# Optimization experiments

Hardware: AMD Instinct MI355X
Metric: run time of the kernel (lower is better)

Reference implementation:

```python
import jax, jax.numpy as jnp
import numpy as np

B, C, T, V = 8, 64, 16, 207
H, WSZ = 8, 4
EPS = 1e-5


def setup_inputs() -> dict:
    key = jax.random.key(0)
    ks = jax.random.split(key, 16)
    def w(k, shape):
        return jax.random.normal(k, shape, jnp.float32) * 0.02
    inp = {"x": jax.random.normal(ks[0], (B, C, T, V), jnp.float32)}
    for i, s in enumerate("ab"):
        o = 1 + i * 4
        inp[f"qkv_w_{s}"] = w(ks[o], (C, 3 * C))
        inp[f"qkv_b_{s}"] = jnp.zeros((3 * C,), jnp.float32)
        inp[f"proj_w_{s}"] = w(ks[o + 1], (C, C))
        inp[f"proj_b_{s}"] = jnp.zeros((C,), jnp.float32)
        inp[f"ffn_w1_{s}"] = w(ks[o + 2], (C, 4 * C))
        inp[f"ffn_b1_{s}"] = jnp.zeros((4 * C,), jnp.float32)
        inp[f"ffn_w2_{s}"] = w(ks[o + 3], (4 * C, C))
        inp[f"ffn_b2_{s}"] = jnp.zeros((C,), jnp.float32)
        inp[f"ln_{s}1_g"] = jnp.ones((C, T, V), jnp.float32)
        inp[f"ln_{s}1_b"] = jnp.zeros((C, T, V), jnp.float32)
        inp[f"ln_{s}2_g"] = jnp.ones((C, T, V), jnp.float32)
        inp[f"ln_{s}2_b"] = jnp.zeros((C, T, V), jnp.float32)
    inp["n_head"] = H
    inp["window_size"] = WSZ
    return inp


def _layer_norm(x, g, b):
    # LayerNorm over (C, T, V) dims of [B, C, T, V]
    mu = jnp.mean(x, axis=(1, 2, 3), keepdims=True)
    var = jnp.var(x, axis=(1, 2, 3), keepdims=True)
    return (x - mu) / jnp.sqrt(var + EPS) * g + b


def _window_att(x, wqkv, bqkv, wo, bo, n_head, wsz):
    # Joint spatio-temporal attention within windows of `wsz` timesteps.
    b_, c_, t_, v_ = x.shape
    nw = t_ // wsz
    dh = c_ // n_head
    # [B,C,T,V] -> [B,T,V,C] -> [B,nW, wsz*V, C]
    xt = jnp.transpose(x, (0, 2, 3, 1)).reshape(b_, nw, wsz * v_, c_)
    qkv = xt @ wqkv + bqkv  # [B,nW,N,3C]
    q, k, v = jnp.split(qkv, 3, axis=-1)
    def heads(t):
        return t.reshape(b_, nw, -1, n_head, dh).transpose(0, 1, 3, 2, 4)  # [B,nW,H,N,dh]
    q, k, v = heads(q), heads(k), heads(v)
    scale = 1.0 / jnp.sqrt(jnp.asarray(dh, jnp.float32))
    att = jax.nn.softmax(jnp.einsum('bwhnd,bwhmd->bwhnm', q, k) * scale, axis=-1)
    out = jnp.einsum('bwhnm,bwhmd->bwhnd', att, v)
    out = out.transpose(0, 1, 3, 2, 4).reshape(b_, nw, wsz * v_, c_) @ wo + bo
    return out.reshape(b_, t_, v_, c_).transpose(0, 3, 1, 2)


def _ffn(x, w1, b1, w2, b2):
    h = jax.nn.relu(jnp.einsum('bctv,cd->bdtv', x, w1) + b1[None, :, None, None])
    return jnp.einsum('bdtv,dc->bctv', h, w2) + b2[None, :, None, None]


def _block(x, wqkv, bqkv, wo, bo, w1, b1, w2, b2, g1, be1, g2, be2, n_head, wsz):
    x = _window_att(x, wqkv, bqkv, wo, bo, n_head, wsz) + x
    x = _layer_norm(x, g1, be1)
    x = _ffn(x, w1, b1, w2, b2) + x
    x = _layer_norm(x, g2, be2)
    # cyclic shift along time by shift_pixel = wsz // 2
    return jnp.roll(x, -(wsz // 2), axis=2)


def reference(x, qkv_w_a, qkv_b_a, proj_w_a, proj_b_a, ffn_w1_a, ffn_b1_a, ffn_w2_a, ffn_b2_a,
              ln_a1_g, ln_a1_b, ln_a2_g, ln_a2_b,
              qkv_w_b, qkv_b_b, proj_w_b, proj_b_b, ffn_w1_b, ffn_b1_b, ffn_w2_b, ffn_b2_b,
              ln_b1_g, ln_b1_b, ln_b2_g, ln_b2_b, n_head, window_size):
    x = _block(x, qkv_w_a, qkv_b_a, proj_w_a, proj_b_a, ffn_w1_a, ffn_b1_a, ffn_w2_a, ffn_b2_a,
               ln_a1_g, ln_a1_b, ln_a2_g, ln_a2_b, n_head, window_size)
    x = _block(x, qkv_w_b, qkv_b_b, proj_w_b, proj_b_b, ffn_w1_b, ffn_b1_b, ffn_w2_b, ffn_b2_b,
               ln_b1_g, ln_b1_b, ln_b2_g, ln_b2_b, n_head, window_size)
    return x
```

## Files before the change

kernel.cpp:

```cpp
#include <hip/hip_runtime.h>
#include <hip/hip_bf16.h>

#define Bb  8
#define Cc  64
#define Tt  16
#define Vv  207
#define Hh  8
#define DH  8
#define NW  4
#define WSZ 4
#define Nn  (WSZ*Vv)
#define NP  832
#define TV  (Tt*Vv)
#define CTV (Cc*Tt*Vv)
#define S   (Bb*CTV)
#define NBWH (Bb*NW*Hh)
#define EPSF 1e-5f
#define QSCALE 0.51006971401146f
#define FRAG_BWH (52*64*4)
#define LAYER_WSZ 49152

typedef __attribute__((ext_vector_type(4))) short bf16x4;
typedef __attribute__((ext_vector_type(4))) float f32x4;
typedef __attribute__((ext_vector_type(2))) unsigned int u32x2;

static __device__ __forceinline__ short f2bf(float f) {
    union { float f; unsigned u; } v; v.f = f;
    unsigned r = (v.u + 0x7FFFu + ((v.u >> 16) & 1u)) >> 16;
    return (short)r;
}

static __device__ __forceinline__ bf16x4 pack4(float a, float b, float c, float d) {
    unsigned ua = __builtin_bit_cast(unsigned, a) + 0x8000u;
    unsigned ub = __builtin_bit_cast(unsigned, b) + 0x8000u;
    unsigned uc = __builtin_bit_cast(unsigned, c) + 0x8000u;
    unsigned ud = __builtin_bit_cast(unsigned, d) + 0x8000u;
    u32x2 t;
    t[0] = (ua >> 16) | (ub & 0xFFFF0000u);
    t[1] = (uc >> 16) | (ud & 0xFFFF0000u);
    return __builtin_bit_cast(bf16x4, t);
}

static __device__ __forceinline__ float pexp2(float x) {
    float t = __builtin_fmaf(x, 0.0558263f, 0.2401536f);
    t = __builtin_fmaf(x, t, 0.6931471f);
    return __builtin_fmaf(x, t, 1.0f);
}

__global__ void prep_w_kernel(const float* __restrict__ qa, const float* __restrict__ pa,
                              const float* __restrict__ w1a, const float* __restrict__ w2a,
                              const float* __restrict__ qbw, const float* __restrict__ pbw,
                              const float* __restrict__ w1b, const float* __restrict__ w2b,
                              short* __restrict__ wf, float* __restrict__ stats) {
    if (blockIdx.x == 0 && threadIdx.x < 64) stats[threadIdx.x] = 0.f;
    int i = blockIdx.x*256 + threadIdx.x;
    int l = i / 12288; int f = i % 12288;
    const float* qw = l ? qbw : qa;
    const float* pw = l ? pbw : pa;
    const float* w1 = l ? w1b : w1a;
    const float* w2 = l ? w2b : w2a;
    short* dst = wf + l*LAYER_WSZ;
    bf16x4 out;
    if (f < 3072) {
        int s = f; int nt = s>>8; int kc = (s>>6)&3; int ln = s&63;
        int li = ln&15; int q = ln>>4;
        #pragma unroll
        for (int j = 0; j < 4; ++j) out[j] = f2bf(qw[(kc*16+q*4+j)*192 + nt*16+li]);
        *((bf16x4*)&dst[s*4]) = out;
    } else if (f < 4096) {
        int s = f-3072; int nt = s>>8; int kc = (s>>6)&3; int ln = s&63;
        int li = ln&15; int q = ln>>4;
        #pragma unroll
        for (int j = 0; j < 4; ++j) out[j] = f2bf(pw[(kc*16+q*4+j)*64 + nt*16+li]);
        *((bf16x4*)&dst[12288 + s*4]) = out;
    } else if (f < 8192) {
        int s = f-4096; int nt = s>>8; int kc = (s>>6)&3; int ln = s&63;
        int li = ln&15; int q = ln>>4;
        #pragma unroll
        for (int j = 0; j < 4; ++j) out[j] = f2bf(w1[(kc*16+q*4+j)*256 + nt*16+li]);
        *((bf16x4*)&dst[16384 + s*4]) = out;
    } else {
        int s = f-8192; int nt = s>>8; int ct = (s>>6)&3; int ln = s&63;
        int li = ln&15; int q = ln>>4;
        #pragma unroll
        for (int j = 0; j < 4; ++j) out[j] = f2bf(w2[(nt*16+q*4+j)*64 + ct*16+li]);
        *((bf16x4*)&dst[32768 + s*4]) = out;
    }
}

__global__ void prep_pads_kernel(short* __restrict__ qf, short* __restrict__ kf,
                                 short* __restrict__ vf) {
    for (int i = blockIdx.x*256 + threadIdx.x; i < NBWH*1664; i += 416*256) {
        int bwh = i / 1664; int rest = i % 1664;
        int nt = rest >> 5; int u = rest & 31;
        size_t base = (size_t)bwh*FRAG_BWH + nt*256;
        *((u32x2*)&qf[base + (32+u)*4]) = (u32x2){0u,0u};
        *((u32x2*)&kf[base + (32+u)*4]) = (u32x2){0u,0u};
        int vlane = (u>>3)*16 + 8 + (u&7);
        short v = ((u&7) == 0) ? (short)0x3F80 : (short)0;
        bf16x4 vv4 = {v,v,v,v};
        *((bf16x4*)&vf[base + vlane*4]) = vv4;
    }
}

__global__ __launch_bounds__(256) void qkv_kernel(const float* __restrict__ src,
        const float* __restrict__ st, const float* __restrict__ g, const float* __restrict__ be,
        const short* __restrict__ wfq, const float* __restrict__ bias,
        short* __restrict__ qf, short* __restrict__ kf, short* __restrict__ vf) {
    __shared__ short wqs[12288];
    __shared__ float bqs[192];
    __shared__ short os[64*196];
    int tid = threadIdx.x;
    int b = blockIdx.x / 52;
    int r0 = (blockIdx.x % 52) * 64;
    const float* xb = src + (size_t)b*CTV;
    {
        const u32x2* wsrc = (const u32x2*)wfq;
        u32x2* wdst = (u32x2*)wqs;
        for (int s = tid; s < 3072; s += 256) wdst[s] = wsrc[s];
    }
    if (tid < 192) bqs[tid] = bias[tid];
    __syncthreads();

    int lane = tid & 63; int wv = tid >> 6;
    int l15 = lane & 15; int quad = lane >> 4;
    int r = r0 + wv*16 + l15;
    int rc = (r < TV) ? r : TV-1;
    int t = rc / Vv; int vv = rc - t*Vv;
    float mean = 0.f, rstd = 0.f; int off;
    if (st) {
        mean = st[b*2] * (1.0f/CTV);
        float var = st[b*2+1] * (1.0f/CTV) - mean*mean;
        rstd = rsqrtf(var + EPSF);
        off = ((t+2)&15)*Vv + vv;
    } else off = rc;

    bf16x4 xf[4];
    #pragma unroll
    for (int kc = 0; kc < 4; ++kc) {
        #pragma unroll
        for (int j = 0; j < 4; ++j) {
            int idx = (kc*16 + quad*4 + j)*TV + off;
            float xv = xb[idx];
            if (st) xv = (xv - mean)*rstd*g[idx] + be[idx];
            xf[kc][j] = f2bf(xv);
        }
    }

    f32x4 accv[12];
    #pragma unroll
    for (int nt = 0; nt < 12; ++nt) {
        float4 bb = *((const float4*)&bqs[nt*16 + quad*4]);
        f32x4 acc = {bb.x, bb.y, bb.z, bb.w};
        #pragma unroll
        for (int kc = 0; kc < 4; ++kc) {
            bf16x4 wf2 = *((const bf16x4*)&wqs[((nt*4 + kc)*64 + lane)*4]);
            acc = __builtin_amdgcn_mfma_f32_16x16x16bf16_1k(wf2, xf[kc], acc, 0, 0, 0);
        }
        accv[nt] = acc;
    }

    int pos = wv*16 + l15;
    #pragma unroll
    for (int nt = 0; nt < 12; ++nt) {
        f32x4 a = accv[nt];
        bf16x4 pk = (nt < 4) ? pack4(a[0]*QSCALE, a[1]*QSCALE, a[2]*QSCALE, a[3]*QSCALE)
                             : pack4(a[0], a[1], a[2], a[3]);
        *((bf16x4*)&os[pos*196 + nt*16 + quad*4]) = pk;
    }
    __syncthreads();

    int pp = tid & 63;
    int rr = r0 + pp;
    bool pv = rr < TV;
    int rrc = pv ? rr : TV-1;
    int t4 = rrc / Vv; int vv4 = rrc - t4*Vv;
    int n2 = (t4 & 3)*Vv + vv4;
    int nt2 = n2 >> 4; int l15n = n2 & 15;
    int quadn = (n2 & 15) >> 2; int jn = n2 & 3;
    int wbase = (b*NW + (t4 >> 2))*Hh;
    if (pv) {
        #pragma unroll
        for (int i = 0; i < 2; ++i) {
            int h = i*4 + wv;
            size_t fb = ((size_t)(wbase+h)*52 + nt2)*256;
            bf16x4 q0 = *((const bf16x4*)&os[pp*196 + h*8]);
            bf16x4 q1 = *((const bf16x4*)&os[pp*196 + h*8 + 4]);
            *((bf16x4*)&qf[fb + l15n*4])        = q0;
            *((bf16x4*)&qf[fb + (16 + l15n)*4]) = q1;
            bf16x4 k0 = *((const bf16x4*)&os[pp*196 + 64 + h*8]);
            bf16x4 k1 = *((const bf16x4*)&os[pp*196 + 64 + h*8 + 4]);
            *((bf16x4*)&kf[fb + l15n*4])        = k0;
            *((bf16x4*)&kf[fb + (16 + l15n)*4]) = k1;
        }
        #pragma unroll
        for (int i = 0; i < 16; ++i) {
            int hd = i*4 + wv;
            int h = hd >> 3; int d = hd & 7;
            vf[(((size_t)(wbase+h)*52 + nt2)*64 + quadn*16 + d)*4 + jn]
                = os[pp*196 + 128 + hd];
        }
    }
}

__global__ __launch_bounds__(1024) void attn_kernel(const short* __restrict__ qf,
        const short* __restrict__ kf, const short* __restrict__ vf,
        short* __restrict__ att) {
    __shared__ short ks2[FRAG_BWH];
    __shared__ short vs2[FRAG_BWH];
    int bwh = blockIdx.x;
    int tid = threadIdx.x;
    int lane = tid & 63;
    int wv = tid >> 6;
    int quad = lane >> 4;
    int l15 = lane & 15;

    {
        const u32x2* kg = (const u32x2*)(kf + (size_t)bwh*FRAG_BWH);
        const u32x2* vg = (const u32x2*)(vf + (size_t)bwh*FRAG_BWH);
        u32x2* kd = (u32x2*)ks2; u32x2* vd = (u32x2*)vs2;
        for (int idx = tid; idx < 3328; idx += 1024) { kd[idx] = kg[idx]; vd[idx] = vg[idx]; }
    }
    __syncthreads();

    int nm = (wv < 4) ? 4 : 3;
    const short* qbase = qf + (size_t)bwh*FRAG_BWH;
    bf16x4 aq[4];
    f32x4 oacc[4];
    #pragma unroll
    for (int i = 0; i < 4; ++i) {
        aq[i] = (bf16x4){0,0,0,0};
        oacc[i] = (f32x4){0.f,0.f,0.f,0.f};
        if (i < nm)
            aq[i] = *(const bf16x4*)(qbase + ((wv + 16*i)*256 + lane*4));
    }

    for (int nt = 0; nt < 52; ++nt) {
        bf16x4 ak = *(const bf16x4*)&ks2[nt*256 + lane*4];
        bf16x4 av = *(const bf16x4*)&vs2[nt*256 + lane*4];
        bool mask = (nt == 51) && (quad == 3);
        #pragma unroll
        for (int i = 0; i < 4; ++i) {
            if (i < nm) {
                f32x4 s = __builtin_amdgcn_mfma_f32_16x16x16bf16_1k(
                              ak, aq[i], (f32x4){0.f,0.f,0.f,0.f}, 0, 0, 0);
                bf16x4 pb = pack4(pexp2(s[0]), pexp2(s[1]), pexp2(s[2]), pexp2(s[3]));
                if (mask) pb = (bf16x4){0,0,0,0};
                oacc[i] = __builtin_amdgcn_mfma_f32_16x16x16bf16_1k(av, pb, oacc[i], 0, 0, 0);
            }
        }
    }
    int h = bwh & 7; int bw = bwh >> 3;
    #pragma unroll
    for (int i = 0; i < 4; ++i) {
        if (i < nm) {
            float ls = __shfl(oacc[i][0], 32 + l15, 64);
            float inv = 1.f / ls;
            int m = (wv + 16*i)*16 + l15;
            if (quad < 2 && m < Nn) {
                bf16x4 ov = pack4(oacc[i][0]*inv, oacc[i][1]*inv,
                                  oacc[i][2]*inv, oacc[i][3]*inv);
                *((bf16x4*)&att[((size_t)bw*Nn + m)*Cc + h*DH + quad*4]) = ov;
            }
        }
    }
}

__global__ __launch_bounds__(256) void proj_kernel(const short* __restrict__ att,
        const short* __restrict__ wfp, const float* __restrict__ bo,
        const float* __restrict__ resid,
        const float* __restrict__ st, const float* __restrict__ g, const float* __restrict__ be,
        float* __restrict__ out, float* __restrict__ stats) {
    __shared__ short wos[4096];
    __shared__ float bos[64];
    __shared__ float r1[256], r2[256];
    int tid = threadIdx.x;
    int b = blockIdx.x / 52;
    int r0 = (blockIdx.x % 52) * 64;
    const float* xb = resid + (size_t)b*CTV;
    {
        const u32x2* wsrc = (const u32x2*)wfp;
        u32x2* wdst = (u32x2*)wos;
        for (int s = tid; s < 1024; s += 256) wdst[s] = wsrc[s];
    }
    if (tid < 64) bos[tid] = bo[tid];
    __syncthreads();

    int lane = tid & 63; int wv = tid >> 6;
    int l15 = lane & 15; int quad = lane >> 4;
    int r = r0 + wv*16 + l15;
    bool valid = r < TV;
    int rc = valid ? r : TV-1;
    int t = rc / Vv; int vv = rc - t*Vv;
    int n = (t & 3)*Vv + vv;
    int bw = b*NW + (t >> 2);
    const short* arow = att + ((size_t)bw*Nn + n)*Cc;
    bf16x4 af[4];
    #pragma unroll
    for (int kc = 0; kc < 4; ++kc)
        af[kc] = *((const bf16x4*)&arow[kc*16 + quad*4]);

    f32x4 acc[4];
    #pragma unroll
    for (int nt = 0; nt < 4; ++nt) {
        float4 bb = *((const float4*)&bos[nt*16 + quad*4]);
        acc[nt] = (f32x4){bb.x, bb.y, bb.z, bb.w};
        #pragma unroll
        for (int kc = 0; kc < 4; ++kc) {
            bf16x4 wf2 = *((const bf16x4*)&wos[((nt*4 + kc)*64 + lane)*4]);
            acc[nt] = __builtin_amdgcn_mfma_f32_16x16x16bf16_1k(wf2, af[kc], acc[nt], 0, 0, 0);
        }
    }
    float mean = 0.f, rstd = 0.f; int off;
    if (st) {
        mean = st[b*2] * (1.0f/CTV);
        float var = st[b*2+1] * (1.0f/CTV) - mean*mean;
        rstd = rsqrtf(var + EPSF);
        off = ((t+2)&15)*Vv + vv;
    } else off = rc;
    float s1 = 0.f, s2 = 0.f;
    if (valid) {
        #pragma unroll
        for (int nt = 0; nt < 4; ++nt) {
            #pragma unroll
            for (int j = 0; j < 4; ++j) {
                int c_out = nt*16 + quad*4 + j;
                int ridx = c_out*TV + off;
                float xv = xb[ridx];
                if (st) xv = (xv - mean)*rstd*g[ridx] + be[ridx];
                float val = acc[nt][j] + xv;
                out[(size_t)b*CTV + (size_t)c_out*TV + r] = val;
                s1 += val; s2 += val*val;
            }
        }
    }
    r1[tid] = s1; r2[tid] = s2;
    __syncthreads();
    for (int o = 128; o > 0; o >>= 1) {
        if (tid < o) { r1[tid] += r1[tid+o]; r2[tid] += r2[tid+o]; }
        __syncthreads();
    }
    if (tid == 0) { atomicAdd(&stats[b*2], r1[0]); atomicAdd(&stats[b*2+1], r2[0]); }
}

__global__ void ln_apply_kernel(const float* __restrict__ x,
                                const float* __restrict__ g,
                                const float* __restrict__ be,
                                const float* __restrict__ stats,
                                float* __restrict__ out,
                                int shift) {
    int idx = blockIdx.x*256 + threadIdx.x;
    if (idx >= S) return;
    int b = idx / CTV; int r = idx % CTV;
    int c = r / TV; int q2 = r % TV; int t = q2 / Vv; int vv = q2 % Vv;
    float mean = stats[b*2] * (1.0f/CTV);
    float var  = stats[b*2+1] * (1.0f/CTV) - mean*mean;
    float rstd = rsqrtf(var + EPSF);
    float val = (x[idx]-mean)*rstd*g[r] + be[r];
    int tout = (t - shift + Tt) % Tt;
    size_t oidx = ((size_t)(b*Cc + c)*Tt + tout)*Vv + vv;
    out[oidx] = val;
}

__global__ __launch_bounds__(256) void ffn_kernel(const float* __restrict__ xin,
        const float* __restrict__ st, const float* __restrict__ g, const float* __restrict__ be,
        const short* __restrict__ wf1, const float* __restrict__ b1,
        const short* __restrict__ wf2g, const float* __restrict__ b2,
        float* __restrict__ out, float* __restrict__ stats) {
    __shared__ short w1s[16384];
    __shared__ short w2s[16384];
    __shared__ short xsf[4096];
    __shared__ float b1s[256];
    __shared__ float b2s[64];
    __shared__ float r1s[256], r2s[256];
    int tid = threadIdx.x;
    int b = blockIdx.x / 52;
    int r0 = (blockIdx.x % 52) * 64;
    const float* xb = xin + (size_t)b*CTV;
    float mean = st[b*2] * (1.0f/CTV);
    float var  = st[b*2+1] * (1.0f/CTV) - mean*mean;
    float rstd = rsqrtf(var + EPSF);

    {
        const u32x2* s1p = (const u32x2*)wf1;
        const u32x2* s2p = (const u32x2*)wf2g;
        u32x2* d1 = (u32x2*)w1s; u32x2* d2 = (u32x2*)w2s;
        for (int s = tid; s < 4096; s += 256) { d1[s] = s1p[s]; d2[s] = s2p[s]; }
    }
    for (int s2 = tid; s2 < 1024; s2 += 256) {
        int wv2 = s2 >> 8; int kc = (s2 >> 6) & 3; int ln = s2 & 63;
        int l15 = ln & 15; int quad = ln >> 4;
        int r = r0 + wv2*16 + l15; if (r >= TV) r = TV-1;
        bf16x4 f;
        #pragma unroll
        for (int j = 0; j < 4; ++j) {
            int idx = (kc*16 + quad*4 + j)*TV + r;
            f[j] = f2bf((xb[idx] - mean)*rstd*g[idx] + be[idx]);
        }
        *((bf16x4*)&xsf[s2*4]) = f;
    }
    b1s[tid] = b1[tid];
    if (tid < 64) b2s[tid] = b2[tid];
    __syncthreads();

    int lane = tid & 63; int wv = tid >> 6;
    int l15 = lane & 15; int quad = lane >> 4;
    bf16x4 xf[4];
    #pragma unroll
    for (int kc = 0; kc < 4; ++kc)
        xf[kc] = *((const bf16x4*)&xsf[((wv*4 + kc)*64 + lane)*4]);

    f32x4 oacc[4];
    #pragma unroll
    for (int ct = 0; ct < 4; ++ct) oacc[ct] = (f32x4){0.f,0.f,0.f,0.f};

    for (int nt = 0; nt < 16; ++nt) {
        float4 bb = *((const float4*)&b1s[nt*16 + quad*4]);
        f32x4 acc = {bb.x, bb.y, bb.z, bb.w};
        #pragma unroll
        for (int kc = 0; kc < 4; ++kc) {
            bf16x4 wfv = *((const bf16x4*)&w1s[((nt*4 + kc)*64 + lane)*4]);
            acc = __builtin_amdgcn_mfma_f32_16x16x16bf16_1k(wfv, xf[kc], acc, 0, 0, 0);
        }
        bf16x4 pf = pack4(fmaxf(acc[0], 0.f), fmaxf(acc[1], 0.f),
                          fmaxf(acc[2], 0.f), fmaxf(acc[3], 0.f));
        #pragma unroll
        for (int ct = 0; ct < 4; ++ct) {
            bf16x4 wfv2 = *((const bf16x4*)&w2s[((nt*4 + ct)*64 + lane)*4]);
            oacc[ct] = __builtin_amdgcn_mfma_f32_16x16x16bf16_1k(wfv2, pf, oacc[ct], 0, 0, 0);
        }
    }
    int r = r0 + wv*16 + l15;
    float s1 = 0.f, s2 = 0.f;
    if (r < TV) {
        #pragma unroll
        for (int ct = 0; ct < 4; ++ct) {
            #pragma unroll
            for (int j = 0; j < 4; ++j) {
                int c_out = ct*16 + quad*4 + j;
                int idx = c_out*TV + r;
                float xv = (xb[idx] - mean)*rstd*g[idx] + be[idx];
                float val = oacc[ct][j] + b2s[c_out] + xv;
                out[(size_t)b*CTV + idx] = val;
                s1 += val; s2 += val*val;
            }
        }
    }
    r1s[tid] = s1; r2s[tid] = s2;
    __syncthreads();
    for (int o = 128; o > 0; o >>= 1) {
        if (tid < o) { r1s[tid] += r1s[tid+o]; r2s[tid] += r2s[tid+o]; }
        __syncthreads();
    }
    if (tid == 0) { atomicAdd(&stats[b*2], r1s[0]); atomicAdd(&stats[b*2+1], r2s[0]); }
}

extern "C" void kernel_launch(void* const* d_in, const int* in_sizes, int n_in,
                              void* d_out, int out_size, void* d_ws, size_t ws_size,
                              hipStream_t stream) {
    const float* xin = (const float*)d_in[0];

    float* bufA  = (float*)d_ws;
    float* bufB  = bufA + S;
    float* stats = bufB + S;
    short* qf    = (short*)(stats + 64);
    short* kf    = qf + (size_t)NBWH*FRAG_BWH;
    short* vf    = kf + (size_t)NBWH*FRAG_BWH;
    short* att   = vf + (size_t)NBWH*FRAG_BWH;
    short* wf    = att + (size_t)32*Nn*64;

    const float* A0  = (const float*)d_in[1];
    const float* A1  = (const float*)d_in[2];
    const float* A2  = (const float*)d_in[3];
    const float* A3  = (const float*)d_in[4];
    const float* A4  = (const float*)d_in[5];
    const float* A5  = (const float*)d_in[6];
    const float* A6  = (const float*)d_in[7];
    const float* A7  = (const float*)d_in[8];
    const float* A8  = (const float*)d_in[9];
    const float* A9  = (const float*)d_in[10];
    const float* A10 = (const float*)d_in[11];
    const float* A11 = (const float*)d_in[12];
    const float* B0  = (const float*)d_in[13];
    const float* B1  = (const float*)d_in[14];
    const float* B2  = (const float*)d_in[15];
    const float* B3  = (const float*)d_in[16];
    const float* B4  = (const float*)d_in[17];
    const float* B5  = (const float*)d_in[18];
    const float* B6  = (const float*)d_in[19];
    const float* B7  = (const float*)d_in[20];
    const float* B8  = (const float*)d_in[21];
    const float* B9  = (const float*)d_in[22];
    const float* B10 = (const float*)d_in[23];
    const float* B11 = (const float*)d_in[24];

    float* st1a = stats + 0;
    float* st2a = stats + 16;
    float* st1b = stats + 32;
    float* st2b = stats + 48;

    short* wfA = wf;
    short* wfB = wf + LAYER_WSZ;

    prep_w_kernel<<<96, 256, 0, stream>>>(A0, A2, A4, A6, B0, B2, B4, B6, wf, stats);
    prep_pads_kernel<<<416, 256, 0, stream>>>(qf, kf, vf);

    qkv_kernel<<<Bb*52, 256, 0, stream>>>(xin, nullptr, nullptr, nullptr,
                                          wfA, A1, qf, kf, vf);
    attn_kernel<<<NBWH, 1024, 0, stream>>>(qf, kf, vf, att);
    proj_kernel<<<Bb*52, 256, 0, stream>>>(att, wfA + 12288, A3, xin,
                                           nullptr, nullptr, nullptr, bufB, st1a);
    ffn_kernel<<<Bb*52, 256, 0, stream>>>(bufB, st1a, A8, A9,
                                          wfA + 16384, A5, wfA + 32768, A7, bufB, st2a);
    qkv_kernel<<<Bb*52, 256, 0, stream>>>(bufB, st2a, A10, A11,
                                          wfB, B1, qf, kf, vf);
    attn_kernel<<<NBWH, 1024, 0, stream>>>(qf, kf, vf, att);
    proj_kernel<<<Bb*52, 256, 0, stream>>>(att, wfB + 12288, B3, bufB,
                                           st2a, A10, A11, bufA, st1b);
    ffn_kernel<<<Bb*52, 256, 0, stream>>>(bufA, st1b, B8, B9,
                                          wfB + 16384, B5, wfB + 32768, B7, bufA, st2b);
    ln_apply_kernel<<<(S+255)/256, 256, 0, stream>>>(bufA, B10, B11, st2b, (float*)d_out, WSZ/2);
}
```

Measured before the change: 310.5 us.

## Fuse all stages into a persistent megakernel with software grid barriers

Result: slower. 438.2 us (+41.1%).

```diff
diff --git a/kernel.cpp b/kernel.cpp
--- a/kernel.cpp
+++ b/kernel.cpp
@@ -19,6 +19,8 @@
 #define QSCALE 0.51006971401146f
 #define FRAG_BWH (52*64*4)
 #define LAYER_WSZ 49152
+#define NBLK 256
+#define SMEM_BYTES 125696
 
 typedef __attribute__((ext_vector_type(4))) short bf16x4;
 typedef __attribute__((ext_vector_type(4))) float f32x4;
@@ -47,50 +49,70 @@
     return __builtin_fmaf(x, t, 1.0f);
 }
 
-__global__ void prep_w_kernel(const float* __restrict__ qa, const float* __restrict__ pa,
-                              const float* __restrict__ w1a, const float* __restrict__ w2a,
-                              const float* __restrict__ qbw, const float* __restrict__ pbw,
-                              const float* __restrict__ w1b, const float* __restrict__ w2b,
-                              short* __restrict__ wf, float* __restrict__ stats) {
-    if (blockIdx.x == 0 && threadIdx.x < 64) stats[threadIdx.x] = 0.f;
-    int i = blockIdx.x*256 + threadIdx.x;
-    int l = i / 12288; int f = i % 12288;
-    const float* qw = l ? qbw : qa;
-    const float* pw = l ? pbw : pa;
-    const float* w1 = l ? w1b : w1a;
-    const float* w2 = l ? w2b : w2a;
-    short* dst = wf + l*LAYER_WSZ;
-    bf16x4 out;
-    if (f < 3072) {
-        int s = f; int nt = s>>8; int kc = (s>>6)&3; int ln = s&63;
-        int li = ln&15; int q = ln>>4;
-        #pragma unroll
-        for (int j = 0; j < 4; ++j) out[j] = f2bf(qw[(kc*16+q*4+j)*192 + nt*16+li]);
-        *((bf16x4*)&dst[s*4]) = out;
-    } else if (f < 4096) {
-        int s = f-3072; int nt = s>>8; int kc = (s>>6)&3; int ln = s&63;
-        int li = ln&15; int q = ln>>4;
-        #pragma unroll
-        for (int j = 0; j < 4; ++j) out[j] = f2bf(pw[(kc*16+q*4+j)*64 + nt*16+li]);
-        *((bf16x4*)&dst[12288 + s*4]) = out;
-    } else if (f < 8192) {
-        int s = f-4096; int nt = s>>8; int kc = (s>>6)&3; int ln = s&63;
-        int li = ln&15; int q = ln>>4;
-        #pragma unroll
-        for (int j = 0; j < 4; ++j) out[j] = f2bf(w1[(kc*16+q*4+j)*256 + nt*16+li]);
-        *((bf16x4*)&dst[16384 + s*4]) = out;
-    } else {
-        int s = f-8192; int nt = s>>8; int ct = (s>>6)&3; int ln = s&63;
-        int li = ln&15; int q = ln>>4;
-        #pragma unroll
-        for (int j = 0; j < 4; ++j) out[j] = f2bf(w2[(nt*16+q*4+j)*64 + ct*16+li]);
-        *((bf16x4*)&dst[32768 + s*4]) = out;
-    }
-}
-
-__global__ void prep_pads_kernel(short* __restrict__ qf, short* __restrict__ kf,
-                                 short* __restrict__ vf) {
-    for (int i = blockIdx.x*256 + threadIdx.x; i < NBWH*1664; i += 416*256) {
+static __device__ __forceinline__ void gsync(unsigned* bar) {
+    __syncthreads();
+    if (threadIdx.x == 0) {
+        __threadfence();
+        unsigned gen = atomicAdd(&bar[1], 0u);
+        unsigned arrived = atomicAdd(&bar[0], 1u) + 1u;
+        if (arrived == (unsigned)NBLK) {
+            atomicExch(&bar[0], 0u);
+            __threadfence();
+            atomicAdd(&bar[1], 1u);
+        } else {
+            while (atomicAdd(&bar[1], 0u) == gen) { __builtin_amdgcn_s_sleep(8); }
+        }
+        __threadfence();
+    }
+    __syncthreads();
+}
+
+__global__ void prep_kernel(const float* __restrict__ qa, const float* __restrict__ pa,
+                            const float* __restrict__ w1a, const float* __restrict__ w2a,
+                            const float* __restrict__ qbw, const float* __restrict__ pbw,
+                            const float* __restrict__ w1b, const float* __restrict__ w2b,
+                            short* __restrict__ wf, float* __restrict__ stats,
+                            unsigned* __restrict__ bar,
+                            short* __restrict__ qf, short* __restrict__ kf,
+                            short* __restrict__ vf) {
+    int i0 = blockIdx.x*256 + threadIdx.x;
+    if (i0 < 64) stats[i0] = 0.f;
+    if (i0 >= 64 && i0 < 80) bar[i0-64] = 0u;
+    for (int i = i0; i < 24576; i += 416*256) {
+        int l = i / 12288; int f = i % 12288;
+        const float* qw = l ? qbw : qa;
+        const float* pw = l ? pbw : pa;
+        const float* w1 = l ? w1b : w1a;
+        const float* w2 = l ? w2b : w2a;
+        short* dst = wf + l*LAYER_WSZ;
+        bf16x4 out;
+        if (f < 3072) {
+            int s = f; int nt = s>>8; int kc = (s>>6)&3; int ln = s&63;
+            int li = ln&15; int q = ln>>4;
+            #pragma unroll
+            for (int j = 0; j < 4; ++j) out[j] = f2bf(qw[(kc*16+q*4+j)*192 + nt*16+li]);
+            *((bf16x4*)&dst[s*4]) = out;
+        } else if (f < 4096) {
+            int s = f-3072; int nt = s>>8; int kc = (s>>6)&3; int ln = s&63;
+            int li = ln&15; int q = ln>>4;
+            #pragma unroll
+            for (int j = 0; j < 4; ++j) out[j] = f2bf(pw[(kc*16+q*4+j)*64 + nt*16+li]);
+            *((bf16x4*)&dst[12288 + s*4]) = out;
+        } else if (f < 8192) {
+            int s = f-4096; int nt = s>>8; int kc = (s>>6)&3; int ln = s&63;
+            int li = ln&15; int q = ln>>4;
+            #pragma unroll
+            for (int j = 0; j < 4; ++j) out[j] = f2bf(w1[(kc*16+q*4+j)*256 + nt*16+li]);
+            *((bf16x4*)&dst[16384 + s*4]) = out;
+        } else {
+            int s = f-8192; int nt = s>>8; int ct = (s>>6)&3; int ln = s&63;
+            int li = ln&15; int q = ln>>4;
+            #pragma unroll
+            for (int j = 0; j < 4; ++j) out[j] = f2bf(w2[(nt*16+q*4+j)*64 + ct*16+li]);
+            *((bf16x4*)&dst[32768 + s*4]) = out;
+        }
+    }
+    for (int i = i0; i < NBWH*1664; i += 416*256) {
         int bwh = i / 1664; int rest = i % 1664;
         int nt = rest >> 5; int u = rest & 31;
         size_t base = (size_t)bwh*FRAG_BWH + nt*256;
@@ -103,118 +125,113 @@
     }
 }
 
-__global__ __launch_bounds__(256) void qkv_kernel(const float* __restrict__ src,
-        const float* __restrict__ st, const float* __restrict__ g, const float* __restrict__ be,
+
+static __device__ __forceinline__ void st_qkv(char* smem, int bid, int tid,
+        const float* __restrict__ src, const float* __restrict__ st,
+        const float* __restrict__ g, const float* __restrict__ be,
         const short* __restrict__ wfq, const float* __restrict__ bias,
         short* __restrict__ qf, short* __restrict__ kf, short* __restrict__ vf) {
-    __shared__ short wqs[12288];
-    __shared__ float bqs[192];
-    __shared__ short os[64*196];
-    int tid = threadIdx.x;
-    int b = blockIdx.x / 52;
-    int r0 = (blockIdx.x % 52) * 64;
-    const float* xb = src + (size_t)b*CTV;
+    short* wqs = (short*)smem;
+    float* bqs = (float*)(smem + 24576);
+    int quarter = tid >> 8; int qtid = tid & 255;
+    short* os = (short*)(smem + 25344) + quarter*12544;
     {
         const u32x2* wsrc = (const u32x2*)wfq;
         u32x2* wdst = (u32x2*)wqs;
-        for (int s = tid; s < 3072; s += 256) wdst[s] = wsrc[s];
-    }
-    if (tid < 192) bqs[tid] = bias[tid];
-    __syncthreads();
-
-    int lane = tid & 63; int wv = tid >> 6;
+        for (int s = tid; s < 3072; s += 1024) wdst[s] = wsrc[s];
+        if (tid < 192) bqs[tid] = bias[tid];
+    }
+    __syncthreads();
+    int qid = bid*4 + quarter;
+    bool vt = qid < 416;
+    int b = vt ? qid/52 : 0;
+    int r0 = vt ? (qid%52)*64 : 0;
+    int lane = qtid & 63; int qwv = qtid >> 6;
     int l15 = lane & 15; int quad = lane >> 4;
-    int r = r0 + wv*16 + l15;
-    int rc = (r < TV) ? r : TV-1;
-    int t = rc / Vv; int vv = rc - t*Vv;
-    float mean = 0.f, rstd = 0.f; int off;
-    if (st) {
-        mean = st[b*2] * (1.0f/CTV);
-        float var = st[b*2+1] * (1.0f/CTV) - mean*mean;
-        rstd = rsqrtf(var + EPSF);
-        off = ((t+2)&15)*Vv + vv;
-    } else off = rc;
-
-    bf16x4 xf[4];
-    #pragma unroll
-    for (int kc = 0; kc < 4; ++kc) {
-        #pragma unroll
-        for (int j = 0; j < 4; ++j) {
-            int idx = (kc*16 + quad*4 + j)*TV + off;
-            float xv = xb[idx];
-            if (st) xv = (xv - mean)*rstd*g[idx] + be[idx];
-            xf[kc][j] = f2bf(xv);
-        }
-    }
-
-    f32x4 accv[12];
-    #pragma unroll
-    for (int nt = 0; nt < 12; ++nt) {
-        float4 bb = *((const float4*)&bqs[nt*16 + quad*4]);
-        f32x4 acc = {bb.x, bb.y, bb.z, bb.w};
+    if (vt) {
+        const float* xb = src + (size_t)b*CTV;
+        int r = r0 + qwv*16 + l15;
+        int rc = (r < TV) ? r : TV-1;
+        int t = rc / Vv; int vv = rc - t*Vv;
+        float mean = 0.f, rstd = 0.f; int off;
+        if (st) {
+            mean = st[b*2] * (1.0f/CTV);
+            float var = st[b*2+1] * (1.0f/CTV) - mean*mean;
+            rstd = rsqrtf(var + EPSF);
+            off = ((t+2)&15)*Vv + vv;
+        } else off = rc;
+        bf16x4 xf[4];
         #pragma unroll
         for (int kc = 0; kc < 4; ++kc) {
-            bf16x4 wf2 = *((const bf16x4*)&wqs[((nt*4 + kc)*64 + lane)*4]);
-            acc = __builtin_amdgcn_mfma_f32_16x16x16bf16_1k(wf2, xf[kc], acc, 0, 0, 0);
-        }
-        accv[nt] = acc;
-    }
-
-    int pos = wv*16 + l15;
-    #pragma unroll
-    for (int nt = 0; nt < 12; ++nt) {
-        f32x4 a = accv[nt];
-        bf16x4 pk = (nt < 4) ? pack4(a[0]*QSCALE, a[1]*QSCALE, a[2]*QSCALE, a[3]*QSCALE)
-                             : pack4(a[0], a[1], a[2], a[3]);
-        *((bf16x4*)&os[pos*196 + nt*16 + quad*4]) = pk;
-    }
-    __syncthreads();
-
-    int pp = tid & 63;
-    int rr = r0 + pp;
-    bool pv = rr < TV;
-    int rrc = pv ? rr : TV-1;
-    int t4 = rrc / Vv; int vv4 = rrc - t4*Vv;
-    int n2 = (t4 & 3)*Vv + vv4;
-    int nt2 = n2 >> 4; int l15n = n2 & 15;
-    int quadn = (n2 & 15) >> 2; int jn = n2 & 3;
-    int wbase = (b*NW + (t4 >> 2))*Hh;
-    if (pv) {
-        #pragma unroll
-        for (int i = 0; i < 2; ++i) {
-            int h = i*4 + wv;
-            size_t fb = ((size_t)(wbase+h)*52 + nt2)*256;
-            bf16x4 q0 = *((const bf16x4*)&os[pp*196 + h*8]);
-            bf16x4 q1 = *((const bf16x4*)&os[pp*196 + h*8 + 4]);
-            *((bf16x4*)&qf[fb + l15n*4])        = q0;
-            *((bf16x4*)&qf[fb + (16 + l15n)*4]) = q1;
-            bf16x4 k0 = *((const bf16x4*)&os[pp*196 + 64 + h*8]);
-            bf16x4 k1 = *((const bf16x4*)&os[pp*196 + 64 + h*8 + 4]);
-            *((bf16x4*)&kf[fb + l15n*4])        = k0;
-            *((bf16x4*)&kf[fb + (16 + l15n)*4]) = k1;
-        }
-        #pragma unroll
-        for (int i = 0; i < 16; ++i) {
-            int hd = i*4 + wv;
-            int h = hd >> 3; int d = hd & 7;
-            vf[(((size_t)(wbase+h)*52 + nt2)*64 + quadn*16 + d)*4 + jn]
-                = os[pp*196 + 128 + hd];
-        }
-    }
-}
-
-__global__ __launch_bounds__(1024) void attn_kernel(const short* __restrict__ qf,
-        const short* __restrict__ kf, const short* __restrict__ vf,
-        short* __restrict__ att) {
-    __shared__ short ks2[FRAG_BWH];
-    __shared__ short vs2[FRAG_BWH];
-    int bwh = blockIdx.x;
-    int tid = threadIdx.x;
+            #pragma unroll
+            for (int j = 0; j < 4; ++j) {
+                int idx = (kc*16 + quad*4 + j)*TV + off;
+                float xv = xb[idx];
+                if (st) xv = (xv - mean)*rstd*g[idx] + be[idx];
+                xf[kc][j] = f2bf(xv);
+            }
+        }
+        int pos = qwv*16 + l15;
+        #pragma unroll
+        for (int nt = 0; nt < 12; ++nt) {
+            float4 bb = *((const float4*)&bqs[nt*16 + quad*4]);
+            f32x4 acc = {bb.x, bb.y, bb.z, bb.w};
+            #pragma unroll
+            for (int kc = 0; kc < 4; ++kc) {
+                bf16x4 wf2 = *((const bf16x4*)&wqs[((nt*4 + kc)*64 + lane)*4]);
+                acc = __builtin_amdgcn_mfma_f32_16x16x16bf16_1k(wf2, xf[kc], acc, 0, 0, 0);
+            }
+            bf16x4 pk = (nt < 4) ? pack4(acc[0]*QSCALE, acc[1]*QSCALE, acc[2]*QSCALE, acc[3]*QSCALE)
+                                 : pack4(acc[0], acc[1], acc[2], acc[3]);
+            *((bf16x4*)&os[pos*196 + nt*16 + quad*4]) = pk;
+        }
+    }
+    __syncthreads();
+    if (vt) {
+        int pp = qtid & 63;
+        int rr = r0 + pp;
+        bool pv = rr < TV;
+        int rrc = pv ? rr : TV-1;
+        int t4 = rrc / Vv; int vv4 = rrc - t4*Vv;
+        int n2 = (t4 & 3)*Vv + vv4;
+        int nt2 = n2 >> 4; int l15n = n2 & 15;
+        int quadn = (n2 & 15) >> 2; int jn = n2 & 3;
+        int wbase = (b*NW + (t4 >> 2))*Hh;
+        if (pv) {
+            #pragma unroll
+            for (int i = 0; i < 2; ++i) {
+                int h = i*4 + qwv;
+                size_t fb = ((size_t)(wbase+h)*52 + nt2)*256;
+                bf16x4 q0 = *((const bf16x4*)&os[pp*196 + h*8]);
+                bf16x4 q1 = *((const bf16x4*)&os[pp*196 + h*8 + 4]);
+                *((bf16x4*)&qf[fb + l15n*4])        = q0;
+                *((bf16x4*)&qf[fb + (16 + l15n)*4]) = q1;
+                bf16x4 k0 = *((const bf16x4*)&os[pp*196 + 64 + h*8]);
+                bf16x4 k1 = *((const bf16x4*)&os[pp*196 + 64 + h*8 + 4]);
+                *((bf16x4*)&kf[fb + l15n*4])        = k0;
+                *((bf16x4*)&kf[fb + (16 + l15n)*4]) = k1;
+            }
+            #pragma unroll
+            for (int i = 0; i < 16; ++i) {
+                int hd = i*4 + qwv;
+                int h = hd >> 3; int d = hd & 7;
+                vf[(((size_t)(wbase+h)*52 + nt2)*64 + quadn*16 + d)*4 + jn]
+                    = os[pp*196 + 128 + hd];
+            }
+        }
+    }
+}
+
+static __device__ __forceinline__ void st_attn(char* smem, int bid, int tid,
+        const short* __restrict__ qf, const short* __restrict__ kf,
+        const short* __restrict__ vf, short* __restrict__ att) {
+    short* ks2 = (short*)smem;
+    short* vs2 = (short*)(smem + 26624);
+    int bwh = bid;
     int lane = tid & 63;
     int wv = tid >> 6;
     int quad = lane >> 4;
     int l15 = lane & 15;
-
     {
         const u32x2* kg = (const u32x2*)(kf + (size_t)bwh*FRAG_BWH);
         const u32x2* vg = (const u32x2*)(vf + (size_t)bwh*FRAG_BWH);
@@ -222,7 +239,6 @@
         for (int idx = tid; idx < 3328; idx += 1024) { kd[idx] = kg[idx]; vd[idx] = vg[idx]; }
     }
     __syncthreads();
-
     int nm = (wv < 4) ? 4 : 3;
     const short* qbase = qf + (size_t)bwh*FRAG_BWH;
     bf16x4 aq[4];
@@ -234,7 +250,6 @@
         if (i < nm)
             aq[i] = *(const bf16x4*)(qbase + ((wv + 16*i)*256 + lane*4));
     }
-
     for (int nt = 0; nt < 52; ++nt) {
         bf16x4 ak = *(const bf16x4*)&ks2[nt*256 + lane*4];
         bf16x4 av = *(const bf16x4*)&vs2[nt*256 + lane*4];
@@ -266,193 +281,239 @@
     }
 }
 
-__global__ __launch_bounds__(256) void proj_kernel(const short* __restrict__ att,
-        const short* __restrict__ wfp, const float* __restrict__ bo,
-        const float* __restrict__ resid,
-        const float* __restrict__ st, const float* __restrict__ g, const float* __restrict__ be,
+static __device__ __forceinline__ void st_proj(char* smem, int bid, int tid,
+        const short* __restrict__ att, const short* __restrict__ wfp,
+        const float* __restrict__ bo, const float* __restrict__ resid,
+        const float* __restrict__ st, const float* __restrict__ g,
+        const float* __restrict__ be,
         float* __restrict__ out, float* __restrict__ stats) {
-    __shared__ short wos[4096];
-    __shared__ float bos[64];
-    __shared__ float r1[256], r2[256];
-    int tid = threadIdx.x;
-    int b = blockIdx.x / 52;
-    int r0 = (blockIdx.x % 52) * 64;
-    const float* xb = resid + (size_t)b*CTV;
+    short* wos = (short*)smem;
+    float* bos = (float*)(smem + 8192);
+    float* redb = (float*)(smem + 8448);
+    int quarter = tid >> 8; int qtid = tid & 255;
+    float* r1 = redb + quarter*512;
+    float* r2 = r1 + 256;
     {
         const u32x2* wsrc = (const u32x2*)wfp;
         u32x2* wdst = (u32x2*)wos;
-        for (int s = tid; s < 1024; s += 256) wdst[s] = wsrc[s];
-    }
-    if (tid < 64) bos[tid] = bo[tid];
-    __syncthreads();
-
-    int lane = tid & 63; int wv = tid >> 6;
+        if (tid < 1024) wdst[tid] = wsrc[tid];
+        if (tid < 64) bos[tid] = bo[tid];
+    }
+    __syncthreads();
+    int qid = bid*4 + quarter;
+    bool vt = qid < 416;
+    int b = vt ? qid/52 : 0;
+    int r0 = vt ? (qid%52)*64 : 0;
+    int lane = qtid & 63; int qwv = qtid >> 6;
     int l15 = lane & 15; int quad = lane >> 4;
-    int r = r0 + wv*16 + l15;
-    bool valid = r < TV;
-    int rc = valid ? r : TV-1;
-    int t = rc / Vv; int vv = rc - t*Vv;
-    int n = (t & 3)*Vv + vv;
-    int bw = b*NW + (t >> 2);
-    const short* arow = att + ((size_t)bw*Nn + n)*Cc;
-    bf16x4 af[4];
-    #pragma unroll
-    for (int kc = 0; kc < 4; ++kc)
-        af[kc] = *((const bf16x4*)&arow[kc*16 + quad*4]);
-
-    f32x4 acc[4];
-    #pragma unroll
-    for (int nt = 0; nt < 4; ++nt) {
-        float4 bb = *((const float4*)&bos[nt*16 + quad*4]);
-        acc[nt] = (f32x4){bb.x, bb.y, bb.z, bb.w};
-        #pragma unroll
-        for (int kc = 0; kc < 4; ++kc) {
-            bf16x4 wf2 = *((const bf16x4*)&wos[((nt*4 + kc)*64 + lane)*4]);
-            acc[nt] = __builtin_amdgcn_mfma_f32_16x16x16bf16_1k(wf2, af[kc], acc[nt], 0, 0, 0);
-        }
-    }
-    float mean = 0.f, rstd = 0.f; int off;
-    if (st) {
-        mean = st[b*2] * (1.0f/CTV);
-        float var = st[b*2+1] * (1.0f/CTV) - mean*mean;
-        rstd = rsqrtf(var + EPSF);
-        off = ((t+2)&15)*Vv + vv;
-    } else off = rc;
     float s1 = 0.f, s2 = 0.f;
-    if (valid) {
+    if (vt) {
+        const float* xb = resid + (size_t)b*CTV;
+        int r = r0 + qwv*16 + l15;
+        bool valid = r < TV;
+        int rc = valid ? r : TV-1;
+        int t = rc / Vv; int vv = rc - t*Vv;
+        int n = (t & 3)*Vv + vv;
+        int bw = b*NW + (t >> 2);
+        const short* arow = att + ((size_t)bw*Nn + n)*Cc;
+        bf16x4 af[4];
+        #pragma unroll
+        for (int kc = 0; kc < 4; ++kc)
+            af[kc] = *((const bf16x4*)&arow[kc*16 + quad*4]);
+        f32x4 acc[4];
         #pragma unroll
         for (int nt = 0; nt < 4; ++nt) {
-            #pragma unroll
-            for (int j = 0; j < 4; ++j) {
-                int c_out = nt*16 + quad*4 + j;
-                int ridx = c_out*TV + off;
-                float xv = xb[ridx];
-                if (st) xv = (xv - mean)*rstd*g[ridx] + be[ridx];
-                float val = acc[nt][j] + xv;
-                out[(size_t)b*CTV + (size_t)c_out*TV + r] = val;
-                s1 += val; s2 += val*val;
-            }
-        }
-    }
-    r1[tid] = s1; r2[tid] = s2;
+            float4 bb = *((const float4*)&bos[nt*16 + quad*4]);
+            acc[nt] = (f32x4){bb.x, bb.y, bb.z, bb.w};
+            #pragma unroll
+            for (int kc = 0; kc < 4; ++kc) {
+                bf16x4 wf2 = *((const bf16x4*)&wos[((nt*4 + kc)*64 + lane)*4]);
+                acc[nt] = __builtin_amdgcn_mfma_f32_16x16x16bf16_1k(wf2, af[kc], acc[nt], 0, 0, 0);
+            }
+        }
+        float mean = 0.f, rstd = 0.f; int off;
+        if (st) {
+            mean = st[b*2] * (1.0f/CTV);
+            float var = st[b*2+1] * (1.0f/CTV) - mean*mean;
+            rstd = rsqrtf(var + EPSF);
+            off = ((t+2)&15)*Vv + vv;
+        } else off = rc;
+        if (valid) {
+            #pragma unroll
+            for (int nt = 0; nt < 4; ++nt) {
+                #pragma unroll
+                for (int j = 0; j < 4; ++j) {
+                    int c_out = nt*16 + quad*4 + j;
+                    int ridx = c_out*TV + off;
+                    float xv = xb[ridx];
+                    if (st) xv = (xv - mean)*rstd*g[ridx] + be[ridx];
+                    float val = acc[nt][j] + xv;
+                    out[(size_t)b*CTV + (size_t)c_out*TV + r] = val;
+                    s1 += val; s2 += val*val;
+                }
+            }
+        }
+    }
+    r1[qtid] = s1; r2[qtid] = s2;
     __syncthreads();
     for (int o = 128; o > 0; o >>= 1) {
-        if (tid < o) { r1[tid] += r1[tid+o]; r2[tid] += r2[tid+o]; }
+        if (qtid < o) { r1[qtid] += r1[qtid+o]; r2[qtid] += r2[qtid+o]; }
         __syncthreads();
     }
-    if (tid == 0) { atomicAdd(&stats[b*2], r1[0]); atomicAdd(&stats[b*2+1], r2[0]); }
-}
-
-__global__ void ln_apply_kernel(const float* __restrict__ x,
-                                const float* __restrict__ g,
-                                const float* __restrict__ be,
-                                const float* __restrict__ stats,
-                                float* __restrict__ out,
-                                int shift) {
-    int idx = blockIdx.x*256 + threadIdx.x;
-    if (idx >= S) return;
-    int b = idx / CTV; int r = idx % CTV;
-    int c = r / TV; int q2 = r % TV; int t = q2 / Vv; int vv = q2 % Vv;
-    float mean = stats[b*2] * (1.0f/CTV);
-    float var  = stats[b*2+1] * (1.0f/CTV) - mean*mean;
-    float rstd = rsqrtf(var + EPSF);
-    float val = (x[idx]-mean)*rstd*g[r] + be[r];
-    int tout = (t - shift + Tt) % Tt;
-    size_t oidx = ((size_t)(b*Cc + c)*Tt + tout)*Vv + vv;
-    out[oidx] = val;
-}
-
-__global__ __launch_bounds__(256) void ffn_kernel(const float* __restrict__ xin,
-        const float* __restrict__ st, const float* __restrict__ g, const float* __restrict__ be,
+    if (qtid == 0 && vt) { atomicAdd(&stats[b*2], r1[0]); atomicAdd(&stats[b*2+1], r2[0]); }
+}
+
+static __device__ __forceinline__ void st_ffn(char* smem, int bid, int tid,
+        const float* __restrict__ xin, const float* __restrict__ st,
+        const float* __restrict__ g, const float* __restrict__ be,
         const short* __restrict__ wf1, const float* __restrict__ b1,
         const short* __restrict__ wf2g, const float* __restrict__ b2,
         float* __restrict__ out, float* __restrict__ stats) {
-    __shared__ short w1s[16384];
-    __shared__ short w2s[16384];
-    __shared__ short xsf[4096];
-    __shared__ float b1s[256];
-    __shared__ float b2s[64];
-    __shared__ float r1s[256], r2s[256];
-    int tid = threadIdx.x;
-    int b = blockIdx.x / 52;
-    int r0 = (blockIdx.x % 52) * 64;
+    short* w1s = (short*)smem;
+    short* w2s = (short*)(smem + 32768);
+    int quarter = tid >> 8; int qtid = tid & 255;
+    short* xsf = (short*)(smem + 65536) + quarter*4096;
+    float* b1s = (float*)(smem + 98304);
+    float* b2s = (float*)(smem + 99328);
+    float* redb = (float*)(smem + 99584);
+    float* r1s = redb + quarter*512;
+    float* r2s = r1s + 256;
+    {
+        const u32x2* s1p = (const u32x2*)wf1;
+        const u32x2* s2p = (const u32x2*)wf2g;
+        u32x2* d1 = (u32x2*)w1s; u32x2* d2 = (u32x2*)w2s;
+        for (int s = tid; s < 4096; s += 1024) { d1[s] = s1p[s]; d2[s] = s2p[s]; }
+        if (tid < 256) b1s[tid] = b1[tid];
+        if (tid < 64) b2s[tid] = b2[tid];
+    }
+    int qid = bid*4 + quarter;
+    bool vt = qid < 416;
+    int b = vt ? qid/52 : 0;
+    int r0 = vt ? (qid%52)*64 : 0;
     const float* xb = xin + (size_t)b*CTV;
     float mean = st[b*2] * (1.0f/CTV);
     float var  = st[b*2+1] * (1.0f/CTV) - mean*mean;
     float rstd = rsqrtf(var + EPSF);
-
-    {
-        const u32x2* s1p = (const u32x2*)wf1;
-        const u32x2* s2p = (const u32x2*)wf2g;
-        u32x2* d1 = (u32x2*)w1s; u32x2* d2 = (u32x2*)w2s;
-        for (int s = tid; s < 4096; s += 256) { d1[s] = s1p[s]; d2[s] = s2p[s]; }
-    }
-    for (int s2 = tid; s2 < 1024; s2 += 256) {
-        int wv2 = s2 >> 8; int kc = (s2 >> 6) & 3; int ln = s2 & 63;
-        int l15 = ln & 15; int quad = ln >> 4;
-        int r = r0 + wv2*16 + l15; if (r >= TV) r = TV-1;
-        bf16x4 f;
-        #pragma unroll
-        for (int j = 0; j < 4; ++j) {
-            int idx = (kc*16 + quad*4 + j)*TV + r;
-            f[j] = f2bf((xb[idx] - mean)*rstd*g[idx] + be[idx]);
-        }
-        *((bf16x4*)&xsf[s2*4]) = f;
-    }
-    b1s[tid] = b1[tid];
-    if (tid < 64) b2s[tid] = b2[tid];
-    __syncthreads();
-
-    int lane = tid & 63; int wv = tid >> 6;
+    if (vt) {
+        for (int s2 = qtid; s2 < 1024; s2 += 256) {
+            int wv2 = s2 >> 8; int kc = (s2 >> 6) & 3; int ln = s2 & 63;
+            int l15 = ln & 15; int quad = ln >> 4;
+            int r = r0 + wv2*16 + l15; if (r >= TV) r = TV-1;
+            bf16x4 f;
+            #pragma unroll
+            for (int j = 0; j < 4; ++j) {
+                int idx = (kc*16 + quad*4 + j)*TV + r;
+                f[j] = f2bf((xb[idx] - mean)*rstd*g[idx] + be[idx]);
+            }
+            *((bf16x4*)&xsf[s2*4]) = f;
+        }
+    }
+    __syncthreads();
+    int lane = qtid & 63; int qwv = qtid >> 6;
     int l15 = lane & 15; int quad = lane >> 4;
-    bf16x4 xf[4];
-    #pragma unroll
-    for (int kc = 0; kc < 4; ++kc)
-        xf[kc] = *((const bf16x4*)&xsf[((wv*4 + kc)*64 + lane)*4]);
-
-    f32x4 oacc[4];
-    #pragma unroll
-    for (int ct = 0; ct < 4; ++ct) oacc[ct] = (f32x4){0.f,0.f,0.f,0.f};
-
-    for (int nt = 0; nt < 16; ++nt) {
-        float4 bb = *((const float4*)&b1s[nt*16 + quad*4]);
-        f32x4 acc = {bb.x, bb.y, bb.z, bb.w};
-        #pragma unroll
-        for (int kc = 0; kc < 4; ++kc) {
-            bf16x4 wfv = *((const bf16x4*)&w1s[((nt*4 + kc)*64 + lane)*4]);
-            acc = __builtin_amdgcn_mfma_f32_16x16x16bf16_1k(wfv, xf[kc], acc, 0, 0, 0);
-        }
-        bf16x4 pf = pack4(fmaxf(acc[0], 0.f), fmaxf(acc[1], 0.f),
-                          fmaxf(acc[2], 0.f), fmaxf(acc[3], 0.f));
-        #pragma unroll
-        for (int ct = 0; ct < 4; ++ct) {
-            bf16x4 wfv2 = *((const bf16x4*)&w2s[((nt*4 + ct)*64 + lane)*4]);
-            oacc[ct] = __builtin_amdgcn_mfma_f32_16x16x16bf16_1k(wfv2, pf, oacc[ct], 0, 0, 0);
-        }
-    }
-    int r = r0 + wv*16 + l15;
-    float s1 = 0.f, s2 = 0.f;
-    if (r < TV) {
-        #pragma unroll
-        for (int ct = 0; ct < 4; ++ct) {
-            #pragma unroll
-            for (int j = 0; j < 4; ++j) {
-                int c_out = ct*16 + quad*4 + j;
-                int idx = c_out*TV + r;
-                float xv = (xb[idx] - mean)*rstd*g[idx] + be[idx];
-                float val = oacc[ct][j] + b2s[c_out] + xv;
-                out[(size_t)b*CTV + idx] = val;
-                s1 += val; s2 += val*val;
-            }
-        }
-    }
-    r1s[tid] = s1; r2s[tid] = s2;
+    float s1 = 0.f, s2v = 0.f;
+    if (vt) {
+        bf16x4 xf[4];
+        #pragma unroll
+        for (int kc = 0; kc < 4; ++kc)
+            xf[kc] = *((const bf16x4*)&xsf[((qwv*4 + kc)*64 + lane)*4]);
+        f32x4 oacc[4];
+        #pragma unroll
+        for (int ct = 0; ct < 4; ++ct) oacc[ct] = (f32x4){0.f,0.f,0.f,0.f};
+        for (int nt = 0; nt < 16; ++nt) {
+            float4 bb = *((const float4*)&b1s[nt*16 + quad*4]);
+            f32x4 acc = {bb.x, bb.y, bb.z, bb.w};
+            #pragma unroll
+            for (int kc = 0; kc < 4; ++kc) {
+                bf16x4 wfv = *((const bf16x4*)&w1s[((nt*4 + kc)*64 + lane)*4]);
+                acc = __builtin_amdgcn_mfma_f32_16x16x16bf16_1k(wfv, xf[kc], acc, 0, 0, 0);
+            }
+            bf16x4 pf = pack4(fmaxf(acc[0], 0.f), fmaxf(acc[1], 0.f),
+                              fmaxf(acc[2], 0.f), fmaxf(acc[3], 0.f));
+            #pragma unroll
+            for (int ct = 0; ct < 4; ++ct) {
+                bf16x4 wfv2 = *((const bf16x4*)&w2s[((nt*4 + ct)*64 + lane)*4]);
+                oacc[ct] = __builtin_amdgcn_mfma_f32_16x16x16bf16_1k(wfv2, pf, oacc[ct], 0, 0, 0);
+            }
+        }
+        int r = r0 + qwv*16 + l15;
+        if (r < TV) {
+            #pragma unroll
+            for (int ct = 0; ct < 4; ++ct) {
+                #pragma unroll
+                for (int j = 0; j < 4; ++j) {
+                    int c_out = ct*16 + quad*4 + j;
+                    int idx = c_out*TV + r;
+                    float xv = (xb[idx] - mean)*rstd*g[idx] + be[idx];
+                    float val = oacc[ct][j] + b2s[c_out] + xv;
+                    out[(size_t)b*CTV + idx] = val;
+                    s1 += val; s2v += val*val;
+                }
+            }
+        }
+    }
+    r1s[qtid] = s1; r2s[qtid] = s2v;
     __syncthreads();
     for (int o = 128; o > 0; o >>= 1) {
-        if (tid < o) { r1s[tid] += r1s[tid+o]; r2s[tid] += r2s[tid+o]; }
+        if (qtid < o) { r1s[qtid] += r1s[qtid+o]; r2s[qtid] += r2s[qtid+o]; }
         __syncthreads();
     }
-    if (tid == 0) { atomicAdd(&stats[b*2], r1s[0]); atomicAdd(&stats[b*2+1], r2s[0]); }
+    if (qtid == 0 && vt) { atomicAdd(&stats[b*2], r1s[0]); atomicAdd(&stats[b*2+1], r2s[0]); }
+}
+
+static __device__ __forceinline__ void st_lnfinal(int bid, int tid,
+        const float* __restrict__ x, const float* __restrict__ g,
+        const float* __restrict__ be, const float* __restrict__ st,
+        float* __restrict__ out) {
+    for (int idx = bid*1024 + tid; idx < S; idx += NBLK*1024) {
+        int b = idx / CTV; int r = idx % CTV;
+        int c = r / TV; int q2 = r % TV; int t = q2 / Vv; int vv = q2 % Vv;
+        float mean = st[b*2] * (1.0f/CTV);
+        float var  = st[b*2+1] * (1.0f/CTV) - mean*mean;
+        float rstd = rsqrtf(var + EPSF);
+        float val = (x[idx]-mean)*rstd*g[r] + be[r];
+        int tout = (t - 2 + Tt) & 15;
+        size_t oidx = ((size_t)(b*Cc + c)*Tt + tout)*Vv + vv;
+        out[oidx] = val;
+    }
+}
+
+__global__ __launch_bounds__(1024) void mega_kernel(
+        const float* __restrict__ xin, float* __restrict__ bufA, float* __restrict__ bufB,
+        float* __restrict__ stats, unsigned* __restrict__ bar,
+        const short* __restrict__ wf, short* __restrict__ qf, short* __restrict__ kf,
+        short* __restrict__ vf, short* __restrict__ att,
+        const float* A1, const float* A3, const float* A5, const float* A7,
+        const float* A8, const float* A9, const float* A10, const float* A11,
+        const float* B1, const float* B3, const float* B5, const float* B7,
+        const float* B8, const float* B9, const float* B10, const float* B11,
+        float* __restrict__ dout) {
+    __shared__ __align__(16) char smem[SMEM_BYTES];
+    int bid = blockIdx.x; int tid = threadIdx.x;
+    const short* wfA = wf;
+    const short* wfB = wf + LAYER_WSZ;
+
+    st_qkv(smem, bid, tid, xin, nullptr, nullptr, nullptr, wfA, A1, qf, kf, vf);
+    gsync(bar);
+    st_attn(smem, bid, tid, qf, kf, vf, att);
+    gsync(bar);
+    st_proj(smem, bid, tid, att, wfA + 12288, A3, xin, nullptr, nullptr, nullptr,
+            bufB, stats + 0);
+    gsync(bar);
+    st_ffn(smem, bid, tid, bufB, stats + 0, A8, A9, wfA + 16384, A5, wfA + 32768, A7,
+           bufB, stats + 16);
+    gsync(bar);
+    st_qkv(smem, bid, tid, bufB, stats + 16, A10, A11, wfB, B1, qf, kf, vf);
+    gsync(bar);
+    st_attn(smem, bid, tid, qf, kf, vf, att);
+    gsync(bar);
+    st_proj(smem, bid, tid, att, wfB + 12288, B3, bufB, stats + 16, A10, A11,
+            bufA, stats + 32);
+    gsync(bar);
+    st_ffn(smem, bid, tid, bufA, stats + 32, B8, B9, wfB + 16384, B5, wfB + 32768, B7,
+           bufA, stats + 48);
+    gsync(bar);
+    st_lnfinal(bid, tid, bufA, B10, B11, stats + 48, dout);
 }
 
 extern "C" void kernel_launch(void* const* d_in, const int* in_sizes, int n_in,
@@ -463,7 +524,8 @@
     float* bufA  = (float*)d_ws;
     float* bufB  = bufA + S;
     float* stats = bufB + S;
-    short* qf    = (short*)(stats + 64);
+    unsigned* bar = (unsigned*)(stats + 64);
+    short* qf    = (short*)(bar + 16);
     short* kf    = qf + (size_t)NBWH*FRAG_BWH;
     short* vf    = kf + (size_t)NBWH*FRAG_BWH;
     short* att   = vf + (size_t)NBWH*FRAG_BWH;
@@ -494,30 +556,11 @@
     const float* B10 = (const float*)d_in[23];
     const float* B11 = (const float*)d_in[24];
 
-    float* st1a = stats + 0;
-    float* st2a = stats + 16;
-    float* st1b = stats + 32;
-    float* st2b = stats + 48;
-
-    short* wfA = wf;
-    short* wfB = wf + LAYER_WSZ;
-
-    prep_w_kernel<<<96, 256, 0, stream>>>(A0, A2, A4, A6, B0, B2, B4, B6, wf, stats);
-    prep_pads_kernel<<<416, 256, 0, stream>>>(qf, kf, vf);
-
-    qkv_kernel<<<Bb*52, 256, 0, stream>>>(xin, nullptr, nullptr, nullptr,
-                                          wfA, A1, qf, kf, vf);
-    attn_kernel<<<NBWH, 1024, 0, stream>>>(qf, kf, vf, att);
-    proj_kernel<<<Bb*52, 256, 0, stream>>>(att, wfA + 12288, A3, xin,
-                                           nullptr, nullptr, nullptr, bufB, st1a);
-    ffn_kernel<<<Bb*52, 256, 0, stream>>>(bufB, st1a, A8, A9,
-                                          wfA + 16384, A5, wfA + 32768, A7, bufB, st2a);
-    qkv_kernel<<<Bb*52, 256, 0, stream>>>(bufB, st2a, A10, A11,
-                                          wfB, B1, qf, kf, vf);
-    attn_kernel<<<NBWH, 1024, 0, stream>>>(qf, kf, vf, att);
-    proj_kernel<<<Bb*52, 256, 0, stream>>>(att, wfB + 12288, B3, bufB,
-                                           st2a, A10, A11, bufA, st1b);
-    ffn_kernel<<<Bb*52, 256, 0, stream>>>(bufA, st1b, B8, B9,
-                                          wfB + 16384, B5, wfB + 32768, B7, bufA, st2b);
-    ln_apply_kernel<<<(S+255)/256, 256, 0, stream>>>(bufA, B10, B11, st2b, (float*)d_out, WSZ/2);
-}
+    prep_kernel<<<416, 256, 0, stream>>>(A0, A2, A4, A6, B0, B2, B4, B6,
+                                         wf, stats, bar, qf, kf, vf);
+    mega_kernel<<<NBLK, 1024, 0, stream>>>(xin, bufA, bufB, stats, bar,
+                                           wf, qf, kf, vf, att,
+                                           A1, A3, A5, A7, A8, A9, A10, A11,
+                                           B1, B3, B5, B7, B8, B9, B10, B11,
+                                           (float*)d_out);
+}
```
